# Kernel tuning notes

Hardware: AMD Instinct MI355X
Metric: run time of the kernel (lower is better)

The kernel has to match this reference:

```python
import jax, jax.numpy as jnp
import numpy as np

B, N, C_Z, H, C_H, W = 1, 192, 128, 4, 32, 16


def _layer_norm(x, w, b, eps=1e-5):
    mu = jnp.mean(x, axis=-1, keepdims=True)
    var = jnp.mean(jnp.square(x - mu), axis=-1, keepdims=True)
    return (x - mu) * jax.lax.rsqrt(var + eps) * w + b


def setup_inputs() -> dict:
    key = jax.random.key(0)
    ks = jax.random.split(key, 10)
    s = 0.02
    return {
        "z": jax.random.normal(ks[0], (B, N, N, C_Z), jnp.float32),
        "mask": jnp.ones((B, N, N), jnp.float32),
        "ln_w": jnp.ones((C_Z,), jnp.float32),
        "ln_b": jnp.zeros((C_Z,), jnp.float32),
        "w_q": jax.random.normal(ks[1], (C_Z, H * C_H), jnp.float32) * s,
        "w_k": jax.random.normal(ks[2], (C_Z, H * C_H), jnp.float32) * s,
        "w_v": jax.random.normal(ks[3], (C_Z, H * C_H), jnp.float32) * s,
        "w_bias": jax.random.normal(ks[4], (C_Z, H), jnp.float32) * s,
        "w_gate": jax.random.normal(ks[5], (C_Z, H * C_H), jnp.float32) * s,
        "b_gate": jnp.ones((H * C_H,), jnp.float32),
        "w_out": jax.random.normal(ks[6], (H * C_H, C_Z), jnp.float32) * s,
        "b_out": jnp.zeros((C_Z,), jnp.float32),
        "window_size": W,
    }


def reference(z, mask, ln_w, ln_b, w_q, w_k, w_v, w_bias, w_gate, b_gate, w_out, b_out, window_size):
    b, n = z.shape[0], z.shape[1]
    h = w_bias.shape[1]
    c = w_q.shape[1] // h
    w = int(window_size)

    zl = _layer_norm(z, ln_w, ln_b)                       # [B,N,N,Cz]
    q = (zl @ w_q).reshape(b, n, n, h, c)                 # [B,I,J,H,c]
    k = (zl @ w_k).reshape(b, n, n, h, c)
    v = (zl @ w_v).reshape(b, n, n, h, c)
    tb = zl @ w_bias                                      # [B,J,K,H] triangle bias

    # sliding window indices along the key axis, centered at each query j
    idx = jnp.arange(n)[:, None] - (w // 2) + jnp.arange(w)[None, :]   # [N,W]
    valid = (idx >= 0) & (idx < n)                                     # [N,W]
    idx_c = jnp.clip(idx, 0, n - 1)

    k_win = k[:, :, idx_c]                                # [B,I,J,W,H,c]
    v_win = v[:, :, idx_c]                                # [B,I,J,W,H,c]
    tb_win = jnp.take_along_axis(tb, idx_c[None, :, :, None], axis=2)  # [B,J,W,H]
    mask_win = mask[:, :, idx_c] * valid[None, None].astype(mask.dtype)  # [B,I,J,W]

    scale = 1.0 / jnp.sqrt(jnp.asarray(c, z.dtype))
    logits = jnp.einsum('bijhc,bijwhc->bijwh', q * scale, k_win)       # [B,I,J,W,H]
    logits = logits + tb_win[:, None]                                  # bias b_{j,k} broadcast over i
    logits = logits + jnp.where(mask_win > 0, 0.0, -1e9)[..., None]
    attn = jax.nn.softmax(logits, axis=3)

    o = jnp.einsum('bijwh,bijwhc->bijhc', attn, v_win)                 # [B,I,J,H,c]
    g = jax.nn.sigmoid(zl @ w_gate + b_gate).reshape(b, n, n, h, c)
    o = (g * o).reshape(b, n, n, h * c)
    return o @ w_out + b_out                                           # [B,I,J,Cz]
```

## Files before the change

kernel.cpp:

```cpp
#include <hip/hip_runtime.h>
#include <hip/hip_bf16.h>

#define N 192
#define CZ 128
#define NH 4
#define CH 32
#define WIN 16
#define NROWS (N*N)

typedef __attribute__((ext_vector_type(8))) short bf16x8;
typedef __attribute__((ext_vector_type(4))) float f32x4;

static __device__ __forceinline__ ushort f2bf(float x){
    union{float f; unsigned u;} a; a.f = x;
    unsigned r = a.u + 0x7fffu + ((a.u>>16)&1u);
    return (ushort)(r>>16);
}
static __device__ __forceinline__ float bf2f(ushort s){
    union{unsigned u; float f;} a; a.u = ((unsigned)s)<<16;
    return a.f;
}

__global__ __launch_bounds__(256) void k_pack(
    const float* __restrict__ wq, const float* __restrict__ wk,
    const float* __restrict__ wv, const float* __restrict__ wg,
    const float* __restrict__ wo, ushort* __restrict__ WP)
{
    const int m = blockIdx.y;
    const float* W = (m==0)?wq:(m==1)?wk:(m==2)?wv:(m==3)?wg:wo;
    const int f = blockIdx.x*256 + threadIdx.x;
    const int nt = f >> 8, ks = (f >> 6) & 3, lane8 = f & 63;
    const int col = nt*16 + (lane8 & 15);
    const int r0  = ks*32 + (lane8 >> 4)*8;
    ushort tmp[8];
    #pragma unroll
    for (int i=0; i<8; i++) tmp[i] = f2bf(W[(size_t)(r0+i)*CZ + col]);
    *(uint4*)(WP + (size_t)m*16384 + (size_t)f*8) = *(uint4*)tmp;
}

__global__ __launch_bounds__(256) void k_tb(
    const float* __restrict__ z, const float* __restrict__ lnw, const float* __restrict__ lnb,
    const float* __restrict__ wbias, float* __restrict__ tb)
{
    const int tid = threadIdx.x;
    const int wave = tid >> 6, lane = tid & 63;
    const int r  = wave*4 + (lane >> 4);
    const int li = lane & 15;
    const int row = blockIdx.x*16 + r;
    const float* zr = z + (size_t)row*CZ + li*8;
    float4 a = ((const float4*)zr)[0];
    float4 b = ((const float4*)zr)[1];
    float s  = a.x+a.y+a.z+a.w + b.x+b.y+b.z+b.w;
    float s2 = a.x*a.x+a.y*a.y+a.z*a.z+a.w*a.w + b.x*b.x+b.y*b.y+b.z*b.z+b.w*b.w;
    #pragma unroll
    for (int off=1; off<16; off<<=1) { s += __shfl_xor(s, off); s2 += __shfl_xor(s2, off); }
    const float mu   = s * (1.f/CZ);
    const float rstd = rsqrtf(s2*(1.f/CZ) - mu*mu + 1e-5f);
    const int c0 = li*8;
    float vals[8] = {a.x,a.y,a.z,a.w,b.x,b.y,b.z,b.w};
    float tbp[4] = {0.f,0.f,0.f,0.f};
    #pragma unroll
    for (int t=0; t<8; t++) {
        const float nv = (vals[t]-mu)*rstd*lnw[c0+t] + lnb[c0+t];
        float4 wb4 = *(const float4*)(wbias + (c0+t)*4);
        tbp[0] += nv*wb4.x; tbp[1] += nv*wb4.y;
        tbp[2] += nv*wb4.z; tbp[3] += nv*wb4.w;
    }
    #pragma unroll
    for (int off=1; off<16; off<<=1) {
        #pragma unroll
        for (int h=0; h<4; h++) tbp[h] += __shfl_xor(tbp[h], off);
    }
    if (li == 0) *(float4*)(tb + (size_t)row*4) = make_float4(tbp[0],tbp[1],tbp[2],tbp[3]);
}

__global__ __launch_bounds__(512, 4) void k_fused(
    const float* __restrict__ z, const float* __restrict__ lnw, const float* __restrict__ lnb,
    const float* __restrict__ mask, const float* __restrict__ tb,
    const ushort* __restrict__ WP, const float* __restrict__ bg,
    const float* __restrict__ bout, float* __restrict__ out)
{
    __shared__ ushort zlds[48][132];
    __shared__ ushort kl[48][NH][40];
    __shared__ ushort vl[48][NH][40];
    __shared__ ushort qb[32][136];
    __shared__ ushort gb[32][136];
    __shared__ float  ml[48];
    ushort (*po)[136] = (ushort (*)[136])&zlds[0][0];

    const int i   = blockIdx.y;
    const int j0  = blockIdx.x * 32;
    const int tid = threadIdx.x;
    const int wid = tid >> 6, lane = tid & 63;
    const int l16 = lane & 15, lk = lane >> 4;

    #pragma unroll
    for (int pass = 0; pass < 2; ++pass) {
        const int r = pass*32 + (tid >> 4);
        if (r < 48) {
            const int li  = tid & 15;
            const int jj  = j0 - 8 + r;
            const int jjc = min(max(jj, 0), N-1);
            const float* zr = z + ((size_t)i*N + jjc)*CZ + li*8;
            float4 a = ((const float4*)zr)[0];
            float4 b = ((const float4*)zr)[1];
            float s  = a.x+a.y+a.z+a.w + b.x+b.y+b.z+b.w;
            float s2 = a.x*a.x+a.y*a.y+a.z*a.z+a.w*a.w + b.x*b.x+b.y*b.y+b.z*b.z+b.w*b.w;
            #pragma unroll
            for (int off=1; off<16; off<<=1) { s += __shfl_xor(s, off); s2 += __shfl_xor(s2, off); }
            const float mu   = s * (1.f/CZ);
            const float rstd = rsqrtf(s2*(1.f/CZ) - mu*mu + 1e-5f);
            const int c0 = li*8;
            float vals[8] = {a.x,a.y,a.z,a.w,b.x,b.y,b.z,b.w};
            uint4 pk; ushort* ph = (ushort*)&pk;
            #pragma unroll
            for (int t=0; t<8; t++)
                ph[t] = f2bf((vals[t]-mu)*rstd*lnw[c0+t] + lnb[c0+t]);
            *(uint4*)&zlds[r][c0] = pk;
        }
    }
    if (tid < 47) {
        const int jj  = j0 - 8 + tid;
        const int jjc = min(max(jj, 0), N-1);
        const bool ok = (jj >= 0) && (jj < N) && (mask[(size_t)i*N + jjc] > 0.f);
        ml[tid] = ok ? 0.f : -1e9f;
    }
    __syncthreads();

    {
        const int cw   = wid & 3;
        const int half = wid >> 2;

        bf16x8 bfrag[2][4];
        auto loadB = [&](int m) {
            #pragma unroll
            for (int nt2=0; nt2<2; nt2++)
                #pragma unroll
                for (int ks=0; ks<4; ks++)
                    bfrag[nt2][ks] = *(const bf16x8*)(WP + (size_t)m*16384 + (cw*2+nt2)*2048 + ks*512 + lane*8);
        };
        auto projKV = [&](int slot0, ushort (*dst)[NH][40]) {
            bf16x8 af[4];
            #pragma unroll
            for (int ks=0; ks<4; ks++)
                af[ks] = *(const bf16x8*)&zlds[slot0 + l16][ks*32 + lk*8];
            #pragma unroll
            for (int nt2=0; nt2<2; nt2++) {
                f32x4 acc = {0.f,0.f,0.f,0.f};
                #pragma unroll
                for (int ks=0; ks<4; ks++)
                    acc = __builtin_amdgcn_mfma_f32_16x16x32_bf16(bfrag[nt2][ks], af[ks], acc, 0, 0, 0);
                uint2 pk2;
                pk2.x = (unsigned)f2bf(acc[0]) | ((unsigned)f2bf(acc[1])<<16);
                pk2.y = (unsigned)f2bf(acc[2]) | ((unsigned)f2bf(acc[3])<<16);
                *(uint2*)&dst[slot0 + l16][cw][nt2*16 + lk*4] = pk2;
            }
        };
        auto projQG = [&](int slot0, ushort (*dst)[136], bool gate) {
            float4 bg4[2];
            if (gate)
                #pragma unroll
                for (int nt2=0; nt2<2; nt2++)
                    bg4[nt2] = *(const float4*)(bg + cw*32 + nt2*16 + lk*4);
            bf16x8 af[4];
            #pragma unroll
            for (int ks=0; ks<4; ks++)
                af[ks] = *(const bf16x8*)&zlds[slot0 + l16][ks*32 + lk*8];
            #pragma unroll
            for (int nt2=0; nt2<2; nt2++) {
                f32x4 acc = {0.f,0.f,0.f,0.f};
                #pragma unroll
                for (int ks=0; ks<4; ks++)
                    acc = __builtin_amdgcn_mfma_f32_16x16x32_bf16(bfrag[nt2][ks], af[ks], acc, 0, 0, 0);
                float v0,v1,v2,v3;
                if (gate) {
                    v0 = 1.f/(1.f + __expf(-(acc[0] + bg4[nt2].x)));
                    v1 = 1.f/(1.f + __expf(-(acc[1] + bg4[nt2].y)));
                    v2 = 1.f/(1.f + __expf(-(acc[2] + bg4[nt2].z)));
                    v3 = 1.f/(1.f + __expf(-(acc[3] + bg4[nt2].w)));
                } else { v0=acc[0]; v1=acc[1]; v2=acc[2]; v3=acc[3]; }
                uint2 pk2;
                pk2.x = (unsigned)f2bf(v0) | ((unsigned)f2bf(v1)<<16);
                pk2.y = (unsigned)f2bf(v2) | ((unsigned)f2bf(v3)<<16);
                *(uint2*)&dst[slot0 - 8 + l16][cw*32 + nt2*16 + lk*4] = pk2;
            }
        };

        if (half == 0) {
            loadB(1); projKV(0, kl); projKV(16, kl); projKV(32, kl);
            loadB(2); projKV(0, vl); projKV(16, vl);
        } else {
            loadB(2); projKV(32, vl);
            loadB(0); projQG(8, qb, false); projQG(24, qb, false);
            loadB(3); projQG(8, gb, true);  projQG(24, gb, true);
        }
    }
    __syncthreads();

    const int cq   = tid & 3;
    const int h    = (tid >> 2) & 3;
    const int jloc = tid >> 4;
    const int j    = j0 + jloc;
    const int c0l  = cq * 8;

    float qv[8];
    {
        uint4 q1 = *(const uint4*)&qb[jloc][h*CH + c0l];
        const ushort* s1 = (const ushort*)&q1;
        #pragma unroll
        for (int t=0; t<8; t++) qv[t] = bf2f(s1[t]);
    }

    const float scale = 0.17677669529663688f;
    float lg[WIN];
    #pragma unroll
    for (int w=0; w<WIN; w++) {
        const int rel = jloc + w;
        float dot = 0.f;
        {
            uint4 kv = *(const uint4*)&kl[rel][h][c0l];
            const ushort* kp = (const ushort*)&kv;
            #pragma unroll
            for (int t=0; t<8; t++) dot += qv[t]*bf2f(kp[t]);
        }
        dot += __shfl_xor(dot, 1);
        dot += __shfl_xor(dot, 2);
        const int jj  = j - 8 + w;
        const int jjc = min(max(jj, 0), N-1);
        lg[w] = dot*scale + tb[((size_t)j*N + jjc)*4 + h] + ml[rel];
    }
    float mx = lg[0];
    #pragma unroll
    for (int w=1; w<WIN; w++) mx = fmaxf(mx, lg[w]);
    float sum = 0.f;
    #pragma unroll
    for (int w=0; w<WIN; w++) { lg[w] = __expf(lg[w]-mx); sum += lg[w]; }
    const float inv = 1.f/sum;

    float o[8];
    #pragma unroll
    for (int c=0; c<8; c++) o[c] = 0.f;
    #pragma unroll
    for (int w=0; w<WIN; w++) {
        const float p   = lg[w]*inv;
        const int   rel = jloc + w;
        uint4 vv = *(const uint4*)&vl[rel][h][c0l];
        const ushort* vp = (const ushort*)&vv;
        #pragma unroll
        for (int t=0; t<8; t++) o[t] += p*bf2f(vp[t]);
    }

    {
        uint4 g1 = *(const uint4*)&gb[jloc][h*CH + c0l];
        const ushort* s1 = (const ushort*)&g1;
        uint4 o1; ushort* p1 = (ushort*)&o1;
        #pragma unroll
        for (int t=0; t<8; t++) p1[t] = f2bf(o[t] * bf2f(s1[t]));
        *(uint4*)&po[jloc][h*CH + c0l] = o1;
    }

    const int rt  = wid >> 2;
    const int cwo = wid & 3;
    bf16x8 bfrag[2][4];
    float4 bo4[2];
    #pragma unroll
    for (int nt2=0; nt2<2; nt2++) {
        #pragma unroll
        for (int ks=0; ks<4; ks++)
            bfrag[nt2][ks] = *(const bf16x8*)(WP + (size_t)4*16384 + (cwo*2+nt2)*2048 + ks*512 + lane*8);
        bo4[nt2] = *(const float4*)(bout + cwo*32 + nt2*16 + lk*4);
    }
    __syncthreads();

    {
        bf16x8 af[4];
        #pragma unroll
        for (int ks=0; ks<4; ks++)
            af[ks] = *(const bf16x8*)&po[rt*16 + l16][ks*32 + lk*8];
        const size_t orow = (size_t)(i*N + j0 + rt*16 + l16)*CZ;
        #pragma unroll
        for (int nt2=0; nt2<2; nt2++) {
            f32x4 acc = {0.f,0.f,0.f,0.f};
            #pragma unroll
            for (int ks=0; ks<4; ks++)
                acc = __builtin_amdgcn_mfma_f32_16x16x32_bf16(bfrag[nt2][ks], af[ks], acc, 0, 0, 0);
            float4 ov;
            ov.x = acc[0] + bo4[nt2].x; ov.y = acc[1] + bo4[nt2].y;
            ov.z = acc[2] + bo4[nt2].z; ov.w = acc[3] + bo4[nt2].w;
            *(float4*)(out + orow + cwo*32 + nt2*16 + lk*4) = ov;
        }
    }
}

extern "C" void kernel_launch(void* const* d_in, const int* in_sizes, int n_in,
                              void* d_out, int out_size, void* d_ws, size_t ws_size,
                              hipStream_t stream)
{
    const float* z    = (const float*)d_in[0];
    const float* mask = (const float*)d_in[1];
    const float* lnw  = (const float*)d_in[2];
    const float* lnb  = (const float*)d_in[3];
    const float* wq   = (const float*)d_in[4];
    const float* wk   = (const float*)d_in[5];
    const float* wv   = (const float*)d_in[6];
    const float* wb   = (const float*)d_in[7];
    const float* wg   = (const float*)d_in[8];
    const float* bg   = (const float*)d_in[9];
    const float* wo   = (const float*)d_in[10];
    const float* bo   = (const float*)d_in[11];

    float*  tb = (float*)d_ws;
    ushort* WP = (ushort*)(tb + (size_t)NROWS*4);
    if (ws_size < (size_t)NROWS*4*sizeof(float) + 5*16384*sizeof(ushort)) return;

    k_pack <<<dim3(8,5), 256, 0, stream>>>(wq, wk, wv, wg, wo, WP);
    k_tb   <<<NROWS/16, 256, 0, stream>>>(z, lnw, lnb, wb, tb);
    k_fused<<<dim3(N/32, N), 512, 0, stream>>>(z, lnw, lnb, mask, tb, WP, bg, bo, (float*)d_out);
}
```

Before: 54.63 us.

## Merge weight pack into triangle-bias kernel and shrink fused kernel LDS footprint

Folds the weight packing kernel into the triangle-bias kernel, so one launch is removed. In the fused kernel, the separate gate LDS buffer is dropped. Gate values are held in registers and later written into the z buffer once z is no longer needed, with padding reduced to 132. The launch bound is raised to 6 blocks per CU to gain occupancy, which risks register spills and adds one extra barrier.

```diff
diff --git a/kernel.cpp b/kernel.cpp
--- a/kernel.cpp
+++ b/kernel.cpp
@@ -21,28 +21,26 @@
     return a.f;
 }
 
-__global__ __launch_bounds__(256) void k_pack(
+__global__ __launch_bounds__(256) void k_tb_pack(
+    const float* __restrict__ z, const float* __restrict__ lnw, const float* __restrict__ lnb,
+    const float* __restrict__ wbias, float* __restrict__ tb,
     const float* __restrict__ wq, const float* __restrict__ wk,
     const float* __restrict__ wv, const float* __restrict__ wg,
     const float* __restrict__ wo, ushort* __restrict__ WP)
 {
-    const int m = blockIdx.y;
-    const float* W = (m==0)?wq:(m==1)?wk:(m==2)?wv:(m==3)?wg:wo;
-    const int f = blockIdx.x*256 + threadIdx.x;
-    const int nt = f >> 8, ks = (f >> 6) & 3, lane8 = f & 63;
-    const int col = nt*16 + (lane8 & 15);
-    const int r0  = ks*32 + (lane8 >> 4)*8;
-    ushort tmp[8];
-    #pragma unroll
-    for (int i=0; i<8; i++) tmp[i] = f2bf(W[(size_t)(r0+i)*CZ + col]);
-    *(uint4*)(WP + (size_t)m*16384 + (size_t)f*8) = *(uint4*)tmp;
-}
-
-__global__ __launch_bounds__(256) void k_tb(
-    const float* __restrict__ z, const float* __restrict__ lnw, const float* __restrict__ lnb,
-    const float* __restrict__ wbias, float* __restrict__ tb)
-{
     const int tid = threadIdx.x;
+    if (blockIdx.x < 40) {
+        const int m = blockIdx.x >> 3;
+        const float* W = (m==0)?wq:(m==1)?wk:(m==2)?wv:(m==3)?wg:wo;
+        const int f = (blockIdx.x & 7)*256 + tid;
+        const int nt = f >> 8, ks = (f >> 6) & 3, lane8 = f & 63;
+        const int col = nt*16 + (lane8 & 15);
+        const int r0  = ks*32 + (lane8 >> 4)*8;
+        ushort tmp[8];
+        #pragma unroll
+        for (int i=0; i<8; i++) tmp[i] = f2bf(W[(size_t)(r0+i)*CZ + col]);
+        *(uint4*)(WP + (size_t)m*16384 + (size_t)f*8) = *(uint4*)tmp;
+    }
     const int wave = tid >> 6, lane = tid & 63;
     const int r  = wave*4 + (lane >> 4);
     const int li = lane & 15;
@@ -74,19 +72,18 @@
     if (li == 0) *(float4*)(tb + (size_t)row*4) = make_float4(tbp[0],tbp[1],tbp[2],tbp[3]);
 }
 
-__global__ __launch_bounds__(512, 4) void k_fused(
+__global__ __launch_bounds__(512, 6) void k_fused(
     const float* __restrict__ z, const float* __restrict__ lnw, const float* __restrict__ lnb,
     const float* __restrict__ mask, const float* __restrict__ tb,
     const ushort* __restrict__ WP, const float* __restrict__ bg,
     const float* __restrict__ bout, float* __restrict__ out)
 {
     __shared__ ushort zlds[48][132];
-    __shared__ ushort kl[48][NH][40];
-    __shared__ ushort vl[48][NH][40];
-    __shared__ ushort qb[32][136];
-    __shared__ ushort gb[32][136];
+    __shared__ ushort kl[48][132];
+    __shared__ ushort vl[48][132];
+    __shared__ ushort qb[32][132];
     __shared__ float  ml[48];
-    ushort (*po)[136] = (ushort (*)[136])&zlds[0][0];
+    ushort (*gpo)[132] = zlds;
 
     const int i   = blockIdx.y;
     const int j0  = blockIdx.x * 32;
@@ -127,6 +124,7 @@
     }
     __syncthreads();
 
+    uint2 gst0[2], gst1[2];
     {
         const int cw   = wid & 3;
         const int half = wid >> 2;
@@ -139,7 +137,7 @@
                 for (int ks=0; ks<4; ks++)
                     bfrag[nt2][ks] = *(const bf16x8*)(WP + (size_t)m*16384 + (cw*2+nt2)*2048 + ks*512 + lane*8);
         };
-        auto projKV = [&](int slot0, ushort (*dst)[NH][40]) {
+        auto projKV = [&](int slot0, ushort (*dst)[132]) {
             bf16x8 af[4];
             #pragma unroll
             for (int ks=0; ks<4; ks++)
@@ -153,15 +151,10 @@
                 uint2 pk2;
                 pk2.x = (unsigned)f2bf(acc[0]) | ((unsigned)f2bf(acc[1])<<16);
                 pk2.y = (unsigned)f2bf(acc[2]) | ((unsigned)f2bf(acc[3])<<16);
-                *(uint2*)&dst[slot0 + l16][cw][nt2*16 + lk*4] = pk2;
+                *(uint2*)&dst[slot0 + l16][cw*32 + nt2*16 + lk*4] = pk2;
             }
         };
-        auto projQG = [&](int slot0, ushort (*dst)[136], bool gate) {
-            float4 bg4[2];
-            if (gate)
-                #pragma unroll
-                for (int nt2=0; nt2<2; nt2++)
-                    bg4[nt2] = *(const float4*)(bg + cw*32 + nt2*16 + lk*4);
+        auto projQ = [&](int slot0) {
             bf16x8 af[4];
             #pragma unroll
             for (int ks=0; ks<4; ks++)
@@ -172,17 +165,35 @@
                 #pragma unroll
                 for (int ks=0; ks<4; ks++)
                     acc = __builtin_amdgcn_mfma_f32_16x16x32_bf16(bfrag[nt2][ks], af[ks], acc, 0, 0, 0);
-                float v0,v1,v2,v3;
-                if (gate) {
-                    v0 = 1.f/(1.f + __expf(-(acc[0] + bg4[nt2].x)));
-                    v1 = 1.f/(1.f + __expf(-(acc[1] + bg4[nt2].y)));
-                    v2 = 1.f/(1.f + __expf(-(acc[2] + bg4[nt2].z)));
-                    v3 = 1.f/(1.f + __expf(-(acc[3] + bg4[nt2].w)));
-                } else { v0=acc[0]; v1=acc[1]; v2=acc[2]; v3=acc[3]; }
+                uint2 pk2;
+                pk2.x = (unsigned)f2bf(acc[0]) | ((unsigned)f2bf(acc[1])<<16);
+                pk2.y = (unsigned)f2bf(acc[2]) | ((unsigned)f2bf(acc[3])<<16);
+                *(uint2*)&qb[slot0 - 8 + l16][cw*32 + nt2*16 + lk*4] = pk2;
+            }
+        };
+        auto projG = [&](int slot0, uint2* gs) {
+            float4 bg4[2];
+            #pragma unroll
+            for (int nt2=0; nt2<2; nt2++)
+                bg4[nt2] = *(const float4*)(bg + cw*32 + nt2*16 + lk*4);
+            bf16x8 af[4];
+            #pragma unroll
+            for (int ks=0; ks<4; ks++)
+                af[ks] = *(const bf16x8*)&zlds[slot0 + l16][ks*32 + lk*8];
+            #pragma unroll
+            for (int nt2=0; nt2<2; nt2++) {
+                f32x4 acc = {0.f,0.f,0.f,0.f};
+                #pragma unroll
+                for (int ks=0; ks<4; ks++)
+                    acc = __builtin_amdgcn_mfma_f32_16x16x32_bf16(bfrag[nt2][ks], af[ks], acc, 0, 0, 0);
+                const float v0 = 1.f/(1.f + __expf(-(acc[0] + bg4[nt2].x)));
+                const float v1 = 1.f/(1.f + __expf(-(acc[1] + bg4[nt2].y)));
+                const float v2 = 1.f/(1.f + __expf(-(acc[2] + bg4[nt2].z)));
+                const float v3 = 1.f/(1.f + __expf(-(acc[3] + bg4[nt2].w)));
                 uint2 pk2;
                 pk2.x = (unsigned)f2bf(v0) | ((unsigned)f2bf(v1)<<16);
                 pk2.y = (unsigned)f2bf(v2) | ((unsigned)f2bf(v3)<<16);
-                *(uint2*)&dst[slot0 - 8 + l16][cw*32 + nt2*16 + lk*4] = pk2;
+                gs[nt2] = pk2;
             }
         };
 
@@ -191,11 +202,18 @@
             loadB(2); projKV(0, vl); projKV(16, vl);
         } else {
             loadB(2); projKV(32, vl);
-            loadB(0); projQG(8, qb, false); projQG(24, qb, false);
-            loadB(3); projQG(8, gb, true);  projQG(24, gb, true);
+            loadB(0); projQ(8); projQ(24);
+            loadB(3); projG(8, gst0); projG(24, gst1);
         }
     }
     __syncthreads();
+    if ((wid >> 2) == 1) {
+        const int cw = wid & 3;
+        *(uint2*)&gpo[l16     ][cw*32      + lk*4] = gst0[0];
+        *(uint2*)&gpo[l16     ][cw*32 + 16 + lk*4] = gst0[1];
+        *(uint2*)&gpo[16 + l16][cw*32      + lk*4] = gst1[0];
+        *(uint2*)&gpo[16 + l16][cw*32 + 16 + lk*4] = gst1[1];
+    }
 
     const int cq   = tid & 3;
     const int h    = (tid >> 2) & 3;
@@ -205,7 +223,7 @@
 
     float qv[8];
     {
-        uint4 q1 = *(const uint4*)&qb[jloc][h*CH + c0l];
+        uint4 q1 = *(const uint4*)&qb[jloc][h*32 + c0l];
         const ushort* s1 = (const ushort*)&q1;
         #pragma unroll
         for (int t=0; t<8; t++) qv[t] = bf2f(s1[t]);
@@ -218,7 +236,7 @@
         const int rel = jloc + w;
         float dot = 0.f;
         {
-            uint4 kv = *(const uint4*)&kl[rel][h][c0l];
+            uint4 kv = *(const uint4*)&kl[rel][h*32 + c0l];
             const ushort* kp = (const ushort*)&kv;
             #pragma unroll
             for (int t=0; t<8; t++) dot += qv[t]*bf2f(kp[t]);
@@ -244,31 +262,32 @@
     for (int w=0; w<WIN; w++) {
         const float p   = lg[w]*inv;
         const int   rel = jloc + w;
-        uint4 vv = *(const uint4*)&vl[rel][h][c0l];
+        uint4 vv = *(const uint4*)&vl[rel][h*32 + c0l];
         const ushort* vp = (const ushort*)&vv;
         #pragma unroll
         for (int t=0; t<8; t++) o[t] += p*bf2f(vp[t]);
     }
 
+    const int rt  = wid >> 2;
+    const int cwo = wid & 3;
+    bf16x8 bf4[2][4];
+    float4 bo4[2];
+    #pragma unroll
+    for (int nt2=0; nt2<2; nt2++) {
+        #pragma unroll
+        for (int ks=0; ks<4; ks++)
+            bf4[nt2][ks] = *(const bf16x8*)(WP + (size_t)4*16384 + (cwo*2+nt2)*2048 + ks*512 + lane*8);
+        bo4[nt2] = *(const float4*)(bout + cwo*32 + nt2*16 + lk*4);
+    }
+    __syncthreads();
+
     {
-        uint4 g1 = *(const uint4*)&gb[jloc][h*CH + c0l];
+        uint4 g1 = *(const uint4*)&gpo[jloc][h*32 + c0l];
         const ushort* s1 = (const ushort*)&g1;
         uint4 o1; ushort* p1 = (ushort*)&o1;
         #pragma unroll
         for (int t=0; t<8; t++) p1[t] = f2bf(o[t] * bf2f(s1[t]));
-        *(uint4*)&po[jloc][h*CH + c0l] = o1;
-    }
-
-    const int rt  = wid >> 2;
-    const int cwo = wid & 3;
-    bf16x8 bfrag[2][4];
-    float4 bo4[2];
-    #pragma unroll
-    for (int nt2=0; nt2<2; nt2++) {
-        #pragma unroll
-        for (int ks=0; ks<4; ks++)
-            bfrag[nt2][ks] = *(const bf16x8*)(WP + (size_t)4*16384 + (cwo*2+nt2)*2048 + ks*512 + lane*8);
-        bo4[nt2] = *(const float4*)(bout + cwo*32 + nt2*16 + lk*4);
+        *(uint4*)&gpo[jloc][h*32 + c0l] = o1;
     }
     __syncthreads();
 
@@ -276,14 +295,14 @@
         bf16x8 af[4];
         #pragma unroll
         for (int ks=0; ks<4; ks++)
-            af[ks] = *(const bf16x8*)&po[rt*16 + l16][ks*32 + lk*8];
+            af[ks] = *(const bf16x8*)&gpo[rt*16 + l16][ks*32 + lk*8];
         const size_t orow = (size_t)(i*N + j0 + rt*16 + l16)*CZ;
         #pragma unroll
         for (int nt2=0; nt2<2; nt2++) {
             f32x4 acc = {0.f,0.f,0.f,0.f};
             #pragma unroll
             for (int ks=0; ks<4; ks++)
-                acc = __builtin_amdgcn_mfma_f32_16x16x32_bf16(bfrag[nt2][ks], af[ks], acc, 0, 0, 0);
+                acc = __builtin_amdgcn_mfma_f32_16x16x32_bf16(bf4[nt2][ks], af[ks], acc, 0, 0, 0);
             float4 ov;
             ov.x = acc[0] + bo4[nt2].x; ov.y = acc[1] + bo4[nt2].y;
             ov.z = acc[2] + bo4[nt2].z; ov.w = acc[3] + bo4[nt2].w;
@@ -313,7 +332,6 @@
     ushort* WP = (ushort*)(tb + (size_t)NROWS*4);
     if (ws_size < (size_t)NROWS*4*sizeof(float) + 5*16384*sizeof(ushort)) return;
 
-    k_pack <<<dim3(8,5), 256, 0, stream>>>(wq, wk, wv, wg, wo, WP);
-    k_tb   <<<NROWS/16, 256, 0, stream>>>(z, lnw, lnb, wb, tb);
-    k_fused<<<dim3(N/32, N), 512, 0, stream>>>(z, lnw, lnb, mask, tb, WP, bg, bo, (float*)d_out);
-}
+    k_tb_pack<<<NROWS/16, 256, 0, stream>>>(z, lnw, lnb, wb, tb, wq, wk, wv, wg, wo, WP);
+    k_fused  <<<dim3(N/32, N), 512, 0, stream>>>(z, lnw, lnb, mask, tb, WP, bg, bo, (float*)d_out);
+}
```

Measured after the change: 64.24 us. 17.6% more time.
